# Performance work log

Hardware: AMD Instinct MI355X
Metric: run time of the kernel (lower is better)

Reference implementation:

```python
import jax, jax.numpy as jnp
import numpy as np

B, C, S = 16, 8, 128
DT, DX, DY = 0.001, 1.0, 1.0
NUM_STEPS = 10
EPS = 1e-6


def _thomas(a, b, c, d):
    """Batched Thomas tridiagonal solve. a,b,c,d: [M,N] rows; solve along N."""
    aT, bT, cT, dT = a.T, b.T, c.T, d.T  # [N, M]
    zero = jnp.zeros_like(dT[0])

    def fwd(carry, inp):
        cs_p, ds_p = carry
        ai, bi, ci, di = inp
        denom = bi - ai * cs_p + EPS  # i=0: cs_p=0 -> denom = b0 + eps (matches torch)
        cs = ci / denom
        ds = (di - ai * ds_p) / denom
        return (cs, ds), (cs, ds)

    _, (c_star, d_star) = jax.lax.scan(fwd, (zero, zero), (aT, bT, cT, dT))

    def bwd(x_next, inp):
        ci, di = inp
        x = di - ci * x_next
        return x, x

    _, xs = jax.lax.scan(bwd, d_star[-1], (c_star[:-1], d_star[:-1]), reverse=True)
    x = jnp.concatenate([xs, d_star[-1:]], axis=0)  # [N, M]
    return x.T


def _diffuse_rows(u2d, coeff):
    """Implicit 1D diffusion along last axis. u2d, coeff: [M,N]."""
    a = -coeff
    c = -coeff
    b = 1.0 + 2.0 * coeff
    b = b.at[:, 0].set(1.0 + coeff[:, 0])
    b = b.at[:, -1].set(1.0 + coeff[:, -1])
    return _thomas(a, b, c, u2d)


def _forward(u, alpha_base, beta_base, alpha_time_coeff, beta_time_coeff, channel_mixing):
    Bb, Cc, H, W = u.shape
    half = DT / 2.0
    t = 0.0
    for _ in range(NUM_STEPS):
        # x half-step (coefficient alpha at time t)
        alpha = jnp.clip(alpha_base + alpha_time_coeff * t, EPS, 10.0)
        u = jnp.einsum('dc,bchw->bdhw', channel_mixing, u)
        uf = u.reshape(Bb * Cc, H, W)
        af = jnp.broadcast_to(alpha[None], (Bb, Cc, H, W)).reshape(Bb * Cc, H, W)
        uf = _diffuse_rows(uf.reshape(-1, W), af.reshape(-1, W) * half / DX**2).reshape(Bb * Cc, H, W)
        t += half
        # y full step (coefficient beta at time t+dt/2)
        beta = jnp.clip(beta_base + beta_time_coeff * t, EPS, 10.0)
        bf = jnp.broadcast_to(beta[None], (Bb, Cc, H, W)).reshape(Bb * Cc, H, W)
        ut = uf.transpose(0, 2, 1).reshape(-1, H)
        bt = bf.transpose(0, 2, 1).reshape(-1, H)
        ut = _diffuse_rows(ut, bt * DT / DY**2)
        uf = ut.reshape(Bb * Cc, W, H).transpose(0, 2, 1)
        t += half
        # x half-step (coefficient alpha at time t+dt)
        alpha = jnp.clip(alpha_base + alpha_time_coeff * t, EPS, 10.0)
        af = jnp.broadcast_to(alpha[None], (Bb, Cc, H, W)).reshape(Bb * Cc, H, W)
        uf = _diffuse_rows(uf.reshape(-1, W), af.reshape(-1, W) * half / DX**2).reshape(Bb * Cc, H, W)
        u = uf.reshape(Bb, Cc, H, W)
    return u


def setup_inputs() -> dict:
    key = jax.random.key(0)
    k_u, k_cm, k_atc, k_btc = jax.random.split(key, 4)
    u = jax.random.normal(k_u, (B, C, S, S), dtype=jnp.float32)
    alpha_base = jnp.ones((C, S, S), dtype=jnp.float32)
    beta_base = jnp.ones((C, S, S), dtype=jnp.float32)
    alpha_time_coeff = jax.random.normal(k_atc, (C, S, S), dtype=jnp.float32) * 0.01
    beta_time_coeff = jax.random.normal(k_btc, (C, S, S), dtype=jnp.float32) * 0.01
    channel_mixing = jnp.eye(C, dtype=jnp.float32) + jax.random.normal(k_cm, (C, C), dtype=jnp.float32) * 0.01
    return {
        'u': u,
        'alpha_base': alpha_base,
        'beta_base': beta_base,
        'alpha_time_coeff': alpha_time_coeff,
        'beta_time_coeff': beta_time_coeff,
        'channel_mixing': channel_mixing,
    }


def reference(u, alpha_base, beta_base, alpha_time_coeff, beta_time_coeff, channel_mixing):
    return _forward(u, alpha_base, beta_base, alpha_time_coeff, beta_time_coeff, channel_mixing)
```

## Files before the change

kernel.cpp:

```cpp
#include <hip/hip_runtime.h>


constexpr int S_ = 128;
constexpr int RS = 129;
constexpr float EPSF = 1e-6f;

constexpr int OFF_A = 0;
constexpr int OFF_B = 12384;
constexpr int OFF_C = 24768;
constexpr int POOL  = 33024;

__device__ __forceinline__ void jrun(const float (&e)[12], const float (&g)[12],
                                     float (&o)[8]) {
    float x1[12];
    #pragma unroll
    for (int i = 1; i <= 10; ++i) x1[i] = fmaf(g[i], e[i - 1] + e[i + 1], e[i]);
    #pragma unroll
    for (int i = 2; i <= 9; ++i) o[i - 2] = fmaf(g[i], x1[i - 1] + x1[i + 1], e[i]);
}

template <bool HEAD, bool TAILMIX>
__global__ __launch_bounds__(512, 2) void step_kernel(
    const float* __restrict__ usrc, float* __restrict__ udst,
    const float* __restrict__ ab, const float* __restrict__ atc,
    const float* __restrict__ bbeta, const float* __restrict__ btc,
    const float* __restrict__ cm, float t_y, float t_x)
{
    __shared__ float sP[POOL];
    const int tid = threadIdx.x;
    const int b   = blockIdx.x >> 4;
    const int h0  = (blockIdx.x & 15) << 3;

    if (HEAD) {
        #pragma unroll
        for (int m = 0; m < 2; ++m) {
            const int col = tid + 512 * m;
            const int c = col >> 7, w = col & 127;
            #pragma unroll
            for (int hh = 0; hh < 12; ++hh) {
                const int gh = h0 - 2 + hh;
                float v = 0.f;
                if (gh >= 0 && gh < S_) v = usrc[((b * 8 + c) * S_ + gh) * S_ + w];
                sP[OFF_A + (c * 12 + hh) * RS + w] = v;
            }
        }
        __syncthreads();
        {
            float M[64];
            #pragma unroll
            for (int i = 0; i < 64; ++i) M[i] = cm[i];
            #pragma unroll
            for (int m = 0; m < 3; ++m) {
                const int p = tid + 512 * m;
                const int hh = p >> 7, w = p & 127;
                float v[8], o[8];
                #pragma unroll
                for (int c = 0; c < 8; ++c) v[c] = sP[OFF_A + (c * 12 + hh) * RS + w];
                #pragma unroll
                for (int dd = 0; dd < 8; ++dd) {
                    float a = 0.f;
                    #pragma unroll
                    for (int c = 0; c < 8; ++c) a = fmaf(M[dd * 8 + c], v[c], a);
                    o[dd] = a;
                }
                #pragma unroll
                for (int c = 0; c < 8; ++c) sP[OFF_A + (c * 12 + hh) * RS + w] = o[c];
            }
        }
        __syncthreads();
        #pragma unroll
        for (int m = 0; m < 3; ++m) {
            const int run = tid + 512 * m;
            const int r96 = run % 96;
            const int wr  = run / 96;
            const int c = r96 / 12, hh = r96 % 12;
            const int gh = h0 - 2 + hh;
            const int w0 = wr * 8;
            const bool rowin = (gh >= 0 && gh < S_);
            float e[12], g[12];
            #pragma unroll
            for (int j = 0; j < 12; ++j) {
                const int wj = w0 - 2 + j;
                const bool win = (wj >= 0 && wj < S_);
                const float dv = win ? sP[OFF_A + r96 * RS + wj] : 0.f;
                float co = 0.f;
                if (rowin && win) {
                    float al = ab[(c * S_ + gh) * S_ + wj];
                    al = fminf(fmaxf(al, EPSF), 10.f);
                    co = al * 0.0005f;
                }
                const float nb = (wj == 0 || wj == S_ - 1) ? 1.f : 2.f;
                const float rb = __builtin_amdgcn_rcpf(fmaf(nb, co, 1.f) + EPSF);
                e[j] = rb * dv; g[j] = rb * co;
            }
            float o[8]; jrun(e, g, o);
            #pragma unroll
            for (int i = 0; i < 8; ++i) sP[OFF_B + r96 * RS + w0 + i] = o[i];
        }
        __syncthreads();
    }

    #pragma unroll
    for (int m = 0; m < 2; ++m) {
        const int col = tid + 512 * m;
        const int c = col >> 7, w = col & 127;
        float e[12], g[12];
        #pragma unroll
        for (int hh = 0; hh < 12; ++hh) {
            const int gh = h0 - 2 + hh;
            const bool inr = (gh >= 0 && gh < S_);
            const int ghc = inr ? gh : 0;
            float dv;
            if (HEAD) dv = sP[OFF_B + (c * 12 + hh) * RS + w];
            else      dv = inr ? usrc[((b * 8 + c) * S_ + ghc) * S_ + w] : 0.f;
            const int gc = (c * S_ + ghc) * S_ + w;
            float be = fmaf(btc[gc], t_y, bbeta[gc]);
            be = fminf(fmaxf(be, EPSF), 10.f);
            const float co = inr ? be * 0.001f : 0.f;
            const float nb = (gh == 0 || gh == S_ - 1) ? 1.f : 2.f;
            const float rb = __builtin_amdgcn_rcpf(fmaf(nb, co, 1.f) + EPSF);
            e[hh] = rb * dv; g[hh] = rb * co;
        }
        float o[8]; jrun(e, g, o);
        #pragma unroll
        for (int i = 0; i < 8; ++i) sP[OFF_A + (c * 8 + i) * RS + w] = o[i];
    }
    #pragma unroll
    for (int m = 0; m < 16; ++m) {
        const int p = tid + 512 * m;
        const int r = p >> 7, w = p & 127;
        const int c = r >> 3, ho = r & 7;
        const int gc = (c * S_ + h0 + ho) * S_ + w;
        float al = fmaf(atc[gc], t_x, ab[gc]);
        al = fminf(fmaxf(al, EPSF), 10.f);
        sP[OFF_C + r * RS + w] = al * 0.0005f;
    }
    __syncthreads();

    float rbk[2][12], gk[2][12], xo[2][8];
    #pragma unroll
    for (int m = 0; m < 2; ++m) {
        const int run = tid + 512 * m;
        const int r = run & 63, wr = run >> 6;
        const int w0 = wr * 8;
        float e[12];
        #pragma unroll
        for (int j = 0; j < 12; ++j) {
            const int wj = w0 - 2 + j;
            const bool win = (wj >= 0 && wj < S_);
            const float co = win ? sP[OFF_C + r * RS + wj] : 0.f;
            const float dv = win ? sP[OFF_A + r * RS + wj] : 0.f;
            const float nb = (wj == 0 || wj == S_ - 1) ? 1.f : 2.f;
            const float rb = __builtin_amdgcn_rcpf(fmaf(nb, co, 1.f) + EPSF);
            rbk[m][j] = rb; gk[m][j] = rb * co;
            e[j] = rb * dv;
        }
        jrun(e, gk[m], xo[m]);
    }

    if (TAILMIX) {
        #pragma unroll
        for (int m = 0; m < 2; ++m) {
            const int run = tid + 512 * m;
            const int r = run & 63, w0 = (run >> 6) * 8;
            #pragma unroll
            for (int i = 0; i < 8; ++i) sP[OFF_B + r * RS + w0 + i] = xo[m][i];
        }
        __syncthreads();
        float M[64];
        #pragma unroll
        for (int i = 0; i < 64; ++i) M[i] = cm[i];
        #pragma unroll
        for (int m = 0; m < 2; ++m) {
            const int p = tid + 512 * m;
            const int ho = p >> 7, w = p & 127;
            float v[8], o[8];
            #pragma unroll
            for (int c = 0; c < 8; ++c) v[c] = sP[OFF_B + (c * 8 + ho) * RS + w];
            #pragma unroll
            for (int dd = 0; dd < 8; ++dd) {
                float a = 0.f;
                #pragma unroll
                for (int c = 0; c < 8; ++c) a = fmaf(M[dd * 8 + c], v[c], a);
                o[dd] = a;
            }
            #pragma unroll
            for (int c = 0; c < 8; ++c) sP[OFF_A + (c * 8 + ho) * RS + w] = o[c];
        }
        __syncthreads();
        #pragma unroll
        for (int m = 0; m < 2; ++m) {
            const int run = tid + 512 * m;
            const int r = run & 63, wr = run >> 6;
            const int w0 = wr * 8;
            const int c = r >> 3, ho = r & 7;
            float e[12];
            #pragma unroll
            for (int j = 0; j < 12; ++j) {
                const int wj = w0 - 2 + j;
                const bool win = (wj >= 0 && wj < S_);
                const float dv = win ? sP[OFF_A + r * RS + wj] : 0.f;
                e[j] = rbk[m][j] * dv;
            }
            float o[8]; jrun(e, gk[m], o);
            float4* dst4 = (float4*)&udst[((b * 8 + c) * S_ + h0 + ho) * S_ + w0];
            dst4[0] = make_float4(o[0], o[1], o[2], o[3]);
            dst4[1] = make_float4(o[4], o[5], o[6], o[7]);
        }
    } else {
        #pragma unroll
        for (int m = 0; m < 2; ++m) {
            const int run = tid + 512 * m;
            const int r = run & 63, wr = run >> 6;
            const int w0 = wr * 8;
            const int c = r >> 3, ho = r & 7;
            float4* dst4 = (float4*)&udst[((b * 8 + c) * S_ + h0 + ho) * S_ + w0];
            dst4[0] = make_float4(xo[m][0], xo[m][1], xo[m][2], xo[m][3]);
            dst4[1] = make_float4(xo[m][4], xo[m][5], xo[m][6], xo[m][7]);
        }
    }
}

extern "C" void kernel_launch(void* const* d_in, const int* in_sizes, int n_in,
                              void* d_out, int out_size, void* d_ws, size_t ws_size,
                              hipStream_t stream) {
    const float* u_in = (const float*)d_in[0];
    const float* ab   = (const float*)d_in[1];
    const float* bbta = (const float*)d_in[2];
    const float* atc  = (const float*)d_in[3];
    const float* btc  = (const float*)d_in[4];
    const float* cm   = (const float*)d_in[5];
    float* uo = (float*)d_out;
    float* uw = (float*)d_ws;

    const dim3 g(256), blk(512);
    const float dt2 = 0.0005f;

    step_kernel<true, true><<<g, blk, 0, stream>>>(u_in, uw, ab, atc, bbta, btc, cm,
                                                   1 * dt2, 2 * dt2);
    const float* src = uw; float* dst = uo;
    for (int k = 1; k <= 8; ++k) {
        step_kernel<false, true><<<g, blk, 0, stream>>>(src, dst, ab, atc, bbta, btc, cm,
                                                        (2 * k + 1) * dt2, (2 * k + 2) * dt2);
        const float* ns = dst; dst = (dst == uo) ? uw : uo; src = ns;
    }
    step_kernel<false, false><<<g, blk, 0, stream>>>(src, dst, ab, atc, bbta, btc, cm,
                                                     19 * dt2, 20 * dt2);
}
```

Baseline: 181.7 us.

## Halve row tile to 4 rows per block with 256-thread blocks

Each block now produces 4 output rows instead of 8, with 512 blocks of 256 threads and a smaller shared-memory pool. The y-direction sweep uses an 8-row halo window with an 8-wide Jacobi helper, and the tail x-sweep recomputes its coefficients instead of keeping them in registers. The goal is more blocks per CU and lower register and LDS pressure. In exchange the halo overhead grows, since 8 rows are loaded for every 4 produced, and global traffic for beta coefficients and u goes up.

```diff
diff --git a/kernel.cpp b/kernel.cpp
--- a/kernel.cpp
+++ b/kernel.cpp
@@ -4,14 +4,14 @@
 constexpr int S_ = 128;
 constexpr int RS = 129;
 constexpr float EPSF = 1e-6f;
+constexpr float DT2 = 0.0005f;
 
 constexpr int OFF_A = 0;
-constexpr int OFF_B = 12384;
-constexpr int OFF_C = 24768;
-constexpr int POOL  = 33024;
-
-__device__ __forceinline__ void jrun(const float (&e)[12], const float (&g)[12],
-                                     float (&o)[8]) {
+constexpr int OFF_C = 64 * RS;
+constexpr int POOLF = OFF_C + 32 * RS;
+
+__device__ __forceinline__ void jrun12(const float (&e)[12], const float (&g)[12],
+                                       float (&o)[8]) {
     float x1[12];
     #pragma unroll
     for (int i = 1; i <= 10; ++i) x1[i] = fmaf(g[i], e[i - 1] + e[i + 1], e[i]);
@@ -19,100 +19,116 @@
     for (int i = 2; i <= 9; ++i) o[i - 2] = fmaf(g[i], x1[i - 1] + x1[i + 1], e[i]);
 }
 
+__device__ __forceinline__ void jrun8(const float (&e)[8], const float (&g)[8],
+                                      float (&o)[4]) {
+    float x1[8];
+    #pragma unroll
+    for (int i = 1; i <= 6; ++i) x1[i] = fmaf(g[i], e[i - 1] + e[i + 1], e[i]);
+    #pragma unroll
+    for (int i = 2; i <= 5; ++i) o[i - 2] = fmaf(g[i], x1[i - 1] + x1[i + 1], e[i]);
+}
+
 template <bool HEAD, bool TAILMIX>
-__global__ __launch_bounds__(512, 2) void step_kernel(
+__global__ __launch_bounds__(256, 4) void step_kernel(
     const float* __restrict__ usrc, float* __restrict__ udst,
     const float* __restrict__ ab, const float* __restrict__ atc,
     const float* __restrict__ bbeta, const float* __restrict__ btc,
     const float* __restrict__ cm, float t_y, float t_x)
 {
-    __shared__ float sP[POOL];
+    __shared__ float sP[POOLF];
     const int tid = threadIdx.x;
-    const int b   = blockIdx.x >> 4;
-    const int h0  = (blockIdx.x & 15) << 3;
+    const int b   = blockIdx.x >> 5;
+    const int h0  = (blockIdx.x & 31) << 2;
+
+    float M[64];
+    #pragma unroll
+    for (int i = 0; i < 64; ++i) M[i] = cm[i];
 
     if (HEAD) {
         #pragma unroll
-        for (int m = 0; m < 2; ++m) {
-            const int col = tid + 512 * m;
+        for (int m = 0; m < 4; ++m) {
+            const int col = tid + 256 * m;
             const int c = col >> 7, w = col & 127;
             #pragma unroll
-            for (int hh = 0; hh < 12; ++hh) {
+            for (int hh = 0; hh < 8; ++hh) {
                 const int gh = h0 - 2 + hh;
                 float v = 0.f;
                 if (gh >= 0 && gh < S_) v = usrc[((b * 8 + c) * S_ + gh) * S_ + w];
-                sP[OFF_A + (c * 12 + hh) * RS + w] = v;
-            }
-        }
-        __syncthreads();
-        {
-            float M[64];
-            #pragma unroll
-            for (int i = 0; i < 64; ++i) M[i] = cm[i];
-            #pragma unroll
-            for (int m = 0; m < 3; ++m) {
-                const int p = tid + 512 * m;
-                const int hh = p >> 7, w = p & 127;
-                float v[8], o[8];
+                sP[OFF_A + (c * 8 + hh) * RS + w] = v;
+            }
+        }
+        __syncthreads();
+        #pragma unroll
+        for (int m = 0; m < 4; ++m) {
+            const int p = tid + 256 * m;
+            const int hh = p >> 7, w = p & 127;
+            float v[8], o[8];
+            #pragma unroll
+            for (int c = 0; c < 8; ++c) v[c] = sP[OFF_A + (c * 8 + hh) * RS + w];
+            #pragma unroll
+            for (int dd = 0; dd < 8; ++dd) {
+                float a = 0.f;
                 #pragma unroll
-                for (int c = 0; c < 8; ++c) v[c] = sP[OFF_A + (c * 12 + hh) * RS + w];
-                #pragma unroll
-                for (int dd = 0; dd < 8; ++dd) {
-                    float a = 0.f;
-                    #pragma unroll
-                    for (int c = 0; c < 8; ++c) a = fmaf(M[dd * 8 + c], v[c], a);
-                    o[dd] = a;
-                }
-                #pragma unroll
-                for (int c = 0; c < 8; ++c) sP[OFF_A + (c * 12 + hh) * RS + w] = o[c];
-            }
-        }
-        __syncthreads();
-        #pragma unroll
-        for (int m = 0; m < 3; ++m) {
-            const int run = tid + 512 * m;
-            const int r96 = run % 96;
-            const int wr  = run / 96;
-            const int c = r96 / 12, hh = r96 % 12;
+                for (int c = 0; c < 8; ++c) a = fmaf(M[dd * 8 + c], v[c], a);
+                o[dd] = a;
+            }
+            #pragma unroll
+            for (int c = 0; c < 8; ++c) sP[OFF_A + (c * 8 + hh) * RS + w] = o[c];
+        }
+        __syncthreads();
+        float xo[4][8];
+        #pragma unroll
+        for (int m = 0; m < 4; ++m) {
+            const int run = tid + 256 * m;
+            const int r = run & 63, w0 = (run >> 6) * 8;
+            const int c = r >> 3, hh = r & 7;
             const int gh = h0 - 2 + hh;
-            const int w0 = wr * 8;
             const bool rowin = (gh >= 0 && gh < S_);
+            const int ghc = min(max(gh, 0), S_ - 1);
             float e[12], g[12];
             #pragma unroll
             for (int j = 0; j < 12; ++j) {
                 const int wj = w0 - 2 + j;
                 const bool win = (wj >= 0 && wj < S_);
-                const float dv = win ? sP[OFF_A + r96 * RS + wj] : 0.f;
-                float co = 0.f;
-                if (rowin && win) {
-                    float al = ab[(c * S_ + gh) * S_ + wj];
-                    al = fminf(fmaxf(al, EPSF), 10.f);
-                    co = al * 0.0005f;
-                }
+                const int wjc = min(max(wj, 0), S_ - 1);
+                float al = ab[(c * S_ + ghc) * S_ + wjc];
+                al = fminf(fmaxf(al, EPSF), 10.f);
+                const float co = (rowin && win) ? al * 0.0005f : 0.f;
+                const float dv = win ? sP[OFF_A + r * RS + wjc] : 0.f;
                 const float nb = (wj == 0 || wj == S_ - 1) ? 1.f : 2.f;
                 const float rb = __builtin_amdgcn_rcpf(fmaf(nb, co, 1.f) + EPSF);
                 e[j] = rb * dv; g[j] = rb * co;
             }
-            float o[8]; jrun(e, g, o);
-            #pragma unroll
-            for (int i = 0; i < 8; ++i) sP[OFF_B + r96 * RS + w0 + i] = o[i];
-        }
-        __syncthreads();
-    }
-
-    #pragma unroll
-    for (int m = 0; m < 2; ++m) {
-        const int col = tid + 512 * m;
+            jrun12(e, g, xo[m]);
+        }
+        __syncthreads();
+        #pragma unroll
+        for (int m = 0; m < 4; ++m) {
+            const int run = tid + 256 * m;
+            const int r = run & 63, w0 = (run >> 6) * 8;
+            #pragma unroll
+            for (int i = 0; i < 8; ++i) sP[OFF_A + r * RS + w0 + i] = xo[m][i];
+        }
+        __syncthreads();
+    }
+
+    float oy[4][4];
+    #pragma unroll
+    for (int m = 0; m < 4; ++m) {
+        const int col = tid + 256 * m;
         const int c = col >> 7, w = col & 127;
-        float e[12], g[12];
-        #pragma unroll
-        for (int hh = 0; hh < 12; ++hh) {
+        float e[8], g[8];
+        #pragma unroll
+        for (int hh = 0; hh < 8; ++hh) {
             const int gh = h0 - 2 + hh;
             const bool inr = (gh >= 0 && gh < S_);
-            const int ghc = inr ? gh : 0;
+            const int ghc = min(max(gh, 0), S_ - 1);
             float dv;
-            if (HEAD) dv = sP[OFF_B + (c * 12 + hh) * RS + w];
-            else      dv = inr ? usrc[((b * 8 + c) * S_ + ghc) * S_ + w] : 0.f;
+            if (HEAD) dv = sP[OFF_A + (c * 8 + hh) * RS + w];
+            else {
+                dv = usrc[((b * 8 + c) * S_ + ghc) * S_ + w];
+                dv = inr ? dv : 0.f;
+            }
             const int gc = (c * S_ + ghc) * S_ + w;
             float be = fmaf(btc[gc], t_y, bbeta[gc]);
             be = fminf(fmaxf(be, EPSF), 10.f);
@@ -121,15 +137,21 @@
             const float rb = __builtin_amdgcn_rcpf(fmaf(nb, co, 1.f) + EPSF);
             e[hh] = rb * dv; g[hh] = rb * co;
         }
-        float o[8]; jrun(e, g, o);
-        #pragma unroll
-        for (int i = 0; i < 8; ++i) sP[OFF_A + (c * 8 + i) * RS + w] = o[i];
+        jrun8(e, g, oy[m]);
+    }
+    if (HEAD) __syncthreads();
+    #pragma unroll
+    for (int m = 0; m < 4; ++m) {
+        const int col = tid + 256 * m;
+        const int c = col >> 7, w = col & 127;
+        #pragma unroll
+        for (int i = 0; i < 4; ++i) sP[OFF_A + (c * 4 + i) * RS + w] = oy[m][i];
     }
     #pragma unroll
     for (int m = 0; m < 16; ++m) {
-        const int p = tid + 512 * m;
+        const int p = tid + 256 * m;
         const int r = p >> 7, w = p & 127;
-        const int c = r >> 3, ho = r & 7;
+        const int c = r >> 2, ho = r & 3;
         const int gc = (c * S_ + h0 + ho) * S_ + w;
         float al = fmaf(atc[gc], t_x, ab[gc]);
         al = fminf(fmaxf(al, EPSF), 10.f);
@@ -137,46 +159,43 @@
     }
     __syncthreads();
 
-    float rbk[2][12], gk[2][12], xo[2][8];
+    float xo[2][8];
     #pragma unroll
     for (int m = 0; m < 2; ++m) {
-        const int run = tid + 512 * m;
-        const int r = run & 63, wr = run >> 6;
-        const int w0 = wr * 8;
-        float e[12];
+        const int run = tid + 256 * m;
+        const int r = run & 31, w0 = (run >> 5) * 8;
+        float e[12], g[12];
         #pragma unroll
         for (int j = 0; j < 12; ++j) {
             const int wj = w0 - 2 + j;
             const bool win = (wj >= 0 && wj < S_);
-            const float co = win ? sP[OFF_C + r * RS + wj] : 0.f;
-            const float dv = win ? sP[OFF_A + r * RS + wj] : 0.f;
+            const int wjc = min(max(wj, 0), S_ - 1);
+            const float co = win ? sP[OFF_C + r * RS + wjc] : 0.f;
+            const float dv = win ? sP[OFF_A + r * RS + wjc] : 0.f;
             const float nb = (wj == 0 || wj == S_ - 1) ? 1.f : 2.f;
             const float rb = __builtin_amdgcn_rcpf(fmaf(nb, co, 1.f) + EPSF);
-            rbk[m][j] = rb; gk[m][j] = rb * co;
-            e[j] = rb * dv;
-        }
-        jrun(e, gk[m], xo[m]);
+            e[j] = rb * dv; g[j] = rb * co;
+        }
+        jrun12(e, g, xo[m]);
     }
 
     if (TAILMIX) {
-        #pragma unroll
-        for (int m = 0; m < 2; ++m) {
-            const int run = tid + 512 * m;
-            const int r = run & 63, w0 = (run >> 6) * 8;
-            #pragma unroll
-            for (int i = 0; i < 8; ++i) sP[OFF_B + r * RS + w0 + i] = xo[m][i];
-        }
-        __syncthreads();
-        float M[64];
-        #pragma unroll
-        for (int i = 0; i < 64; ++i) M[i] = cm[i];
-        #pragma unroll
-        for (int m = 0; m < 2; ++m) {
-            const int p = tid + 512 * m;
+        __syncthreads();
+        #pragma unroll
+        for (int m = 0; m < 2; ++m) {
+            const int run = tid + 256 * m;
+            const int r = run & 31, w0 = (run >> 5) * 8;
+            #pragma unroll
+            for (int i = 0; i < 8; ++i) sP[OFF_A + r * RS + w0 + i] = xo[m][i];
+        }
+        __syncthreads();
+        #pragma unroll
+        for (int m = 0; m < 2; ++m) {
+            const int p = tid + 256 * m;
             const int ho = p >> 7, w = p & 127;
             float v[8], o[8];
             #pragma unroll
-            for (int c = 0; c < 8; ++c) v[c] = sP[OFF_B + (c * 8 + ho) * RS + w];
+            for (int c = 0; c < 8; ++c) v[c] = sP[OFF_A + (c * 4 + ho) * RS + w];
             #pragma unroll
             for (int dd = 0; dd < 8; ++dd) {
                 float a = 0.f;
@@ -185,24 +204,27 @@
                 o[dd] = a;
             }
             #pragma unroll
-            for (int c = 0; c < 8; ++c) sP[OFF_A + (c * 8 + ho) * RS + w] = o[c];
-        }
-        __syncthreads();
-        #pragma unroll
-        for (int m = 0; m < 2; ++m) {
-            const int run = tid + 512 * m;
-            const int r = run & 63, wr = run >> 6;
-            const int w0 = wr * 8;
-            const int c = r >> 3, ho = r & 7;
-            float e[12];
+            for (int c = 0; c < 8; ++c) sP[OFF_A + (c * 4 + ho) * RS + w] = o[c];
+        }
+        __syncthreads();
+        #pragma unroll
+        for (int m = 0; m < 2; ++m) {
+            const int run = tid + 256 * m;
+            const int r = run & 31, w0 = (run >> 5) * 8;
+            const int c = r >> 2, ho = r & 3;
+            float e[12], g[12];
             #pragma unroll
             for (int j = 0; j < 12; ++j) {
                 const int wj = w0 - 2 + j;
                 const bool win = (wj >= 0 && wj < S_);
-                const float dv = win ? sP[OFF_A + r * RS + wj] : 0.f;
-                e[j] = rbk[m][j] * dv;
-            }
-            float o[8]; jrun(e, gk[m], o);
+                const int wjc = min(max(wj, 0), S_ - 1);
+                const float co = win ? sP[OFF_C + r * RS + wjc] : 0.f;
+                const float dv = win ? sP[OFF_A + r * RS + wjc] : 0.f;
+                const float nb = (wj == 0 || wj == S_ - 1) ? 1.f : 2.f;
+                const float rb = __builtin_amdgcn_rcpf(fmaf(nb, co, 1.f) + EPSF);
+                e[j] = rb * dv; g[j] = rb * co;
+            }
+            float o[8]; jrun12(e, g, o);
             float4* dst4 = (float4*)&udst[((b * 8 + c) * S_ + h0 + ho) * S_ + w0];
             dst4[0] = make_float4(o[0], o[1], o[2], o[3]);
             dst4[1] = make_float4(o[4], o[5], o[6], o[7]);
@@ -210,10 +232,9 @@
     } else {
         #pragma unroll
         for (int m = 0; m < 2; ++m) {
-            const int run = tid + 512 * m;
-            const int r = run & 63, wr = run >> 6;
-            const int w0 = wr * 8;
-            const int c = r >> 3, ho = r & 7;
+            const int run = tid + 256 * m;
+            const int r = run & 31, w0 = (run >> 5) * 8;
+            const int c = r >> 2, ho = r & 3;
             float4* dst4 = (float4*)&udst[((b * 8 + c) * S_ + h0 + ho) * S_ + w0];
             dst4[0] = make_float4(xo[m][0], xo[m][1], xo[m][2], xo[m][3]);
             dst4[1] = make_float4(xo[m][4], xo[m][5], xo[m][6], xo[m][7]);
@@ -233,17 +254,16 @@
     float* uo = (float*)d_out;
     float* uw = (float*)d_ws;
 
-    const dim3 g(256), blk(512);
-    const float dt2 = 0.0005f;
+    const dim3 g(512), blk(256);
 
     step_kernel<true, true><<<g, blk, 0, stream>>>(u_in, uw, ab, atc, bbta, btc, cm,
-                                                   1 * dt2, 2 * dt2);
+                                                   1 * DT2, 2 * DT2);
     const float* src = uw; float* dst = uo;
     for (int k = 1; k <= 8; ++k) {
         step_kernel<false, true><<<g, blk, 0, stream>>>(src, dst, ab, atc, bbta, btc, cm,
-                                                        (2 * k + 1) * dt2, (2 * k + 2) * dt2);
+                                                        (2 * k + 1) * DT2, (2 * k + 2) * DT2);
         const float* ns = dst; dst = (dst == uo) ? uw : uo; src = ns;
     }
     step_kernel<false, false><<<g, blk, 0, stream>>>(src, dst, ab, atc, bbta, btc, cm,
-                                                     19 * dt2, 20 * dt2);
-}
+                                                     19 * DT2, 20 * DT2);
+}
```

After: 194.9 us. 1.07x slower.
